# Performance work log

Measured on AMD Instinct MI355X. Metric: run time of the kernel, lower is better.

The kernel has to match this reference:

```python
import jax, jax.numpy as jnp
import numpy as np

LN_EPS = 1e-5
ATTN_THRESH = 0.0005


def _layernorm(x, g, b):
    mu = jnp.mean(x, axis=-1, keepdims=True)
    var = jnp.mean((x - mu) ** 2, axis=-1, keepdims=True)
    return (x - mu) / jnp.sqrt(var + LN_EPS) * g + b


def setup_inputs() -> dict:
    key = jax.random.key(0)
    ks = jax.random.split(key, 10)
    B, P, X, C = 4, 1024, 8192, 1024
    return {
        "feat": jax.random.normal(ks[0], (B, P, C), dtype=jnp.float32),
        "mem_k": jax.random.normal(ks[1], (B, X, C), dtype=jnp.float32),
        "mem_v": jax.random.normal(ks[2], (B, X, C), dtype=jnp.float32),
        "mem_c": jax.random.uniform(ks[3], (B, X, 1), dtype=jnp.float32),
        "mem_attn": jnp.zeros((B, X, 1), dtype=jnp.float32),
        "g_q": jax.random.uniform(ks[4], (C,), dtype=jnp.float32, minval=0.5, maxval=1.5),
        "b_q": jax.random.normal(ks[5], (C,), dtype=jnp.float32) * 0.02,
        "g_k": jax.random.uniform(ks[6], (C,), dtype=jnp.float32, minval=0.5, maxval=1.5),
        "b_k": jax.random.normal(ks[7], (C,), dtype=jnp.float32) * 0.02,
        "g_v": jax.random.uniform(ks[8], (C,), dtype=jnp.float32, minval=0.5, maxval=1.5),
        "b_v": jax.random.normal(ks[9], (C,), dtype=jnp.float32) * 0.02,
    }


def reference(feat, mem_k, mem_v, mem_c, mem_attn, g_q, b_q, g_k, b_k, g_v, b_v):
    # SpatialMemory.memory_read with res=True
    C = feat.shape[-1]
    q = _layernorm(feat, g_q, b_q)                      # [B,P,C]
    k = _layernorm(mem_k, g_k, b_k)                     # [B,X,C]
    affinity = jnp.einsum('bpc,bxc->bpx', q, k)
    affinity = affinity / jnp.sqrt(jnp.asarray(C, jnp.float32))
    # confidence scaling: mem_c viewed as [B,1,X]
    affinity = affinity * jnp.swapaxes(mem_c, 1, 2)
    attn = jax.nn.softmax(affinity, axis=-1)            # [B,P,X]
    # threshold sparsify + renormalize
    attn = jnp.where(attn < ATTN_THRESH, jnp.zeros((), attn.dtype), attn)
    attn = attn / jnp.sum(attn, axis=-1, keepdims=True)
    v = _layernorm(mem_v, g_v, b_v)                     # [B,X,C]
    out = jnp.einsum('bpx,bxc->bpc', attn, v) + feat    # residual
    return out
```

## Files before the change

### kernel.cpp

```cpp
#include <hip/hip_runtime.h>

typedef __attribute__((ext_vector_type(8))) _Float16 half8;
typedef __attribute__((ext_vector_type(4))) _Float16 half4v;
typedef __attribute__((ext_vector_type(4))) float f32x4;

__device__ __forceinline__ void gll16(const void* g, void* l) {
  __builtin_amdgcn_global_load_lds(
      (const __attribute__((address_space(1))) unsigned int*)g,
      (__attribute__((address_space(3))) unsigned int*)l, 16, 0, 0);
}

__global__ __launch_bounds__(256) void ln_fused(
    const float* __restrict__ feat, const float* __restrict__ mem_k,
    const float* __restrict__ mem_v, const float* __restrict__ g_q,
    const float* __restrict__ b_q, const float* __restrict__ g_k,
    const float* __restrict__ b_k, const float* __restrict__ g_v,
    const float* __restrict__ b_v, _Float16* __restrict__ q16,
    _Float16* __restrict__ k16, char* __restrict__ v8,
    float* __restrict__ vscale) {
  const int C = 1024;
  int wave = threadIdx.x >> 6, lane = threadIdx.x & 63;
  int task = blockIdx.x * 4 + wave;

  const float *x, *g, *b;
  int mode;
  size_t row;
  if (task < 4096) {
    x = feat; g = g_q; b = b_q; mode = 0; row = task;
  } else if (task < 36864) {
    x = mem_k; g = g_k; b = b_k; mode = 1; row = task - 4096;
  } else {
    x = mem_v; g = g_v; b = b_v; mode = 2; row = task - 36864;
  }

  const float4* xr = (const float4*)(x + row * C);
  float4 v[4];
  float s = 0.f, s2 = 0.f;
#pragma unroll
  for (int j = 0; j < 4; ++j) {
    v[j] = xr[lane + j * 64];
    s += v[j].x + v[j].y + v[j].z + v[j].w;
    s2 += v[j].x * v[j].x + v[j].y * v[j].y + v[j].z * v[j].z + v[j].w * v[j].w;
  }
#pragma unroll
  for (int off = 1; off < 64; off <<= 1) {
    s += __shfl_xor(s, off, 64);
    s2 += __shfl_xor(s2, off, 64);
  }
  float mu = s * (1.0f / C);
  float var = s2 * (1.0f / C) - mu * mu;
  float rstd = rsqrtf(var + 1e-5f);

  float y[16];
#pragma unroll
  for (int j = 0; j < 4; ++j) {
    float4 gv = ((const float4*)g)[lane + j * 64];
    float4 bv = ((const float4*)b)[lane + j * 64];
    y[4 * j + 0] = (v[j].x - mu) * rstd * gv.x + bv.x;
    y[4 * j + 1] = (v[j].y - mu) * rstd * gv.y + bv.y;
    y[4 * j + 2] = (v[j].z - mu) * rstd * gv.z + bv.z;
    y[4 * j + 3] = (v[j].w - mu) * rstd * gv.w + bv.w;
  }

  if (mode < 2) {
    _Float16* yo = (mode == 0 ? q16 : k16) + row * C;
#pragma unroll
    for (int j = 0; j < 4; ++j) {
      half4v h;
      h.x = (_Float16)y[4 * j + 0];
      h.y = (_Float16)y[4 * j + 1];
      h.z = (_Float16)y[4 * j + 2];
      h.w = (_Float16)y[4 * j + 3];
      ((half4v*)yo)[lane + j * 64] = h;
    }
  } else {
    float mx = 0.f;
#pragma unroll
    for (int i = 0; i < 16; ++i) mx = fmaxf(mx, fabsf(y[i]));
#pragma unroll
    for (int off = 1; off < 64; off <<= 1) mx = fmaxf(mx, __shfl_xor(mx, off, 64));
    mx = fmaxf(mx, 1e-20f);
    float inv = 127.0f / mx;
    unsigned* yo = (unsigned*)(v8 + row * C);
#pragma unroll
    for (int j = 0; j < 4; ++j) {
      int q0 = (int)rintf(y[4 * j + 0] * inv), q1 = (int)rintf(y[4 * j + 1] * inv);
      int q2 = (int)rintf(y[4 * j + 2] * inv), q3 = (int)rintf(y[4 * j + 3] * inv);
      unsigned pk = ((unsigned)(q0 & 0xff)) | ((unsigned)(q1 & 0xff) << 8) |
                    ((unsigned)(q2 & 0xff) << 16) | ((unsigned)(q3 & 0xff) << 24);
      yo[lane + j * 64] = pk;
    }
    if (lane == 0) vscale[row] = mx * (1.0f / 127.0f);
  }
}

__global__ __launch_bounds__(512, 2) void gemm_qk_256(
    const _Float16* __restrict__ A,
    const _Float16* __restrict__ Bm,
    _Float16* __restrict__ Sm,
    const float* __restrict__ conf)
{
  const int N = 8192, K = 1024;
  int bz = blockIdx.z;
  const _Float16* Ab = A + (size_t)bz * 1024 * K;
  const _Float16* Bb = Bm + (size_t)bz * (size_t)N * K;
  _Float16* Sb = Sm + (size_t)bz * 1024 * N;

  __shared__ _Float16 lA[4 * 8192];
  __shared__ _Float16 lB[4 * 8192];

  int tid = threadIdx.x;
  int wave = tid >> 6, lane = tid & 63;
  int wm = wave >> 2, wn = wave & 3;
  int lr = lane & 31, lk = lane >> 5;
  int m0 = blockIdx.y * 256, n0 = blockIdx.x * 256;

  typedef __attribute__((ext_vector_type(16))) float f32x16;
  f32x16 acc[4][2];
#pragma unroll
  for (int i = 0; i < 4; ++i)
#pragma unroll
    for (int j = 0; j < 2; ++j)
#pragma unroll
      for (int e = 0; e < 16; ++e) acc[i][j][e] = 0.f;

  int r = tid & 255, c0 = tid >> 8;
  const _Float16* gA = Ab + (size_t)(m0 + r) * K + c0 * 8;
  const _Float16* gB = Bb + (size_t)(n0 + r) * K + c0 * 8;
  int dA = c0 * 2048 + r * 8;

  auto stage = [&](int t) {
    int bo = (t & 3) * 8192;
    const _Float16* ga = gA + t * 32;
    const _Float16* gb = gB + t * 32;
    gll16(ga, &lA[bo + dA]);
    gll16(ga + 16, &lA[bo + dA + 4096]);
    gll16(gb, &lB[bo + dA]);
    gll16(gb + 16, &lB[bo + dA + 4096]);
  };

  auto compute = [&](int bo) {
#pragma unroll
    for (int ks = 0; ks < 2; ++ks) {
      const _Float16* la = &lA[bo + (ks * 2 + lk) * 2048 + (wm * 128 + lr) * 8];
      const _Float16* lb = &lB[bo + (ks * 2 + lk) * 2048 + (wn * 64 + lr) * 8];
      half8 a0 = *(const half8*)(la);
      half8 a1 = *(const half8*)(la + 256);
      half8 a2 = *(const half8*)(la + 512);
      half8 a3 = *(const half8*)(la + 768);
      half8 b0 = *(const half8*)(lb);
      half8 b1 = *(const half8*)(lb + 256);
      __builtin_amdgcn_s_setprio(1);
      acc[0][0] = __builtin_amdgcn_mfma_f32_32x32x16_f16(a0, b0, acc[0][0], 0, 0, 0);
      acc[1][0] = __builtin_amdgcn_mfma_f32_32x32x16_f16(a1, b0, acc[1][0], 0, 0, 0);
      acc[2][0] = __builtin_amdgcn_mfma_f32_32x32x16_f16(a2, b0, acc[2][0], 0, 0, 0);
      acc[3][0] = __builtin_amdgcn_mfma_f32_32x32x16_f16(a3, b0, acc[3][0], 0, 0, 0);
      acc[0][1] = __builtin_amdgcn_mfma_f32_32x32x16_f16(a0, b1, acc[0][1], 0, 0, 0);
      acc[1][1] = __builtin_amdgcn_mfma_f32_32x32x16_f16(a1, b1, acc[1][1], 0, 0, 0);
      acc[2][1] = __builtin_amdgcn_mfma_f32_32x32x16_f16(a2, b1, acc[2][1], 0, 0, 0);
      acc[3][1] = __builtin_amdgcn_mfma_f32_32x32x16_f16(a3, b1, acc[3][1], 0, 0, 0);
      __builtin_amdgcn_s_setprio(0);
    }
  };

  stage(0);
  stage(1);
  stage(2);

#pragma unroll 4
  for (int kt = 0; kt < 29; ++kt) {
    stage(kt + 3);
    __builtin_amdgcn_s_waitcnt(0xF7C);
    __builtin_amdgcn_s_barrier();
    __builtin_amdgcn_sched_barrier(0);
    compute((kt & 3) * 8192);
    __builtin_amdgcn_sched_barrier(0);
    __builtin_amdgcn_s_barrier();
  }
  __builtin_amdgcn_s_waitcnt(0xF78);
  __builtin_amdgcn_s_barrier();
  __builtin_amdgcn_sched_barrier(0);
  compute(1 * 8192);
  __builtin_amdgcn_sched_barrier(0);
  __builtin_amdgcn_s_barrier();
  __builtin_amdgcn_s_waitcnt(0xF74);
  __builtin_amdgcn_s_barrier();
  __builtin_amdgcn_sched_barrier(0);
  compute(2 * 8192);
  __builtin_amdgcn_sched_barrier(0);
  __builtin_amdgcn_s_barrier();
  __builtin_amdgcn_s_waitcnt(0xF70);
  __builtin_amdgcn_s_barrier();
  __builtin_amdgcn_sched_barrier(0);
  compute(3 * 8192);

  const float* cb = conf + (size_t)bz * N;
#pragma unroll
  for (int nf = 0; nf < 2; ++nf) {
    int gn = n0 + wn * 64 + nf * 32 + lr;
    float cs = 0.03125f * cb[gn];
#pragma unroll
    for (int mf = 0; mf < 4; ++mf) {
      int gmb = m0 + wm * 128 + mf * 32 + 4 * lk;
#pragma unroll
      for (int rr = 0; rr < 16; ++rr) {
        int gm = gmb + (rr & 3) + 8 * (rr >> 2);
        Sb[(size_t)gm * N + gn] = (_Float16)(acc[mf][nf][rr] * cs);
      }
    }
  }
}

__device__ __forceinline__ void acc4(float* a, unsigned w, float wt) {
  a[0] += wt * (float)(signed char)(w & 0xff);
  a[1] += wt * (float)(signed char)((w >> 8) & 0xff);
  a[2] += wt * (float)(signed char)((w >> 16) & 0xff);
  a[3] += wt * (float)(signed char)(w >> 24);
}

__global__ __launch_bounds__(512) void softmax_gather(
    const _Float16* __restrict__ S, const char* __restrict__ v8,
    const float* __restrict__ vscale, const float* __restrict__ feat,
    float* __restrict__ out) {
  const int X = 8192, C = 1024;
  int row = blockIdx.x;
  int b = row >> 10;
  int t = threadIdx.x;
  int wave = t >> 6, lane = t & 63;

  __shared__ float sh[8];
  __shared__ int scnt;
  __shared__ unsigned short sx[2048];
  __shared__ float sw[2048];
  __shared__ float red[8][1028];

  const half8* sr = (const half8*)(S + (size_t)row * X);
  float v[16];
#pragma unroll
  for (int j = 0; j < 2; ++j) {
    half8 h = sr[t + j * 512];
#pragma unroll
    for (int c = 0; c < 8; ++c) v[j * 8 + c] = (float)h[c];
  }

  float m = -1e30f;
#pragma unroll
  for (int i = 0; i < 16; ++i) m = fmaxf(m, v[i]);
#pragma unroll
  for (int off = 1; off < 64; off <<= 1) m = fmaxf(m, __shfl_xor(m, off, 64));
  if (lane == 0) sh[wave] = m;
  __syncthreads();
  m = fmaxf(fmaxf(fmaxf(sh[0], sh[1]), fmaxf(sh[2], sh[3])),
            fmaxf(fmaxf(sh[4], sh[5]), fmaxf(sh[6], sh[7])));
  __syncthreads();

  float l = 0.f;
#pragma unroll
  for (int i = 0; i < 16; ++i) {
    v[i] = __expf(v[i] - m);
    l += v[i];
  }
#pragma unroll
  for (int off = 1; off < 64; off <<= 1) l += __shfl_xor(l, off, 64);
  if (lane == 0) sh[wave] = l;
  __syncthreads();
  l = sh[0] + sh[1] + sh[2] + sh[3] + sh[4] + sh[5] + sh[6] + sh[7];
  __syncthreads();

  float thr = 0.0005f * l;
  float ks = 0.f;
#pragma unroll
  for (int i = 0; i < 16; ++i) {
    v[i] = (v[i] >= thr) ? v[i] : 0.f;
    ks += v[i];
  }
#pragma unroll
  for (int off = 1; off < 64; off <<= 1) ks += __shfl_xor(ks, off, 64);
  if (lane == 0) sh[wave] = ks;
  if (t == 0) scnt = 0;
  __syncthreads();
  ks = sh[0] + sh[1] + sh[2] + sh[3] + sh[4] + sh[5] + sh[6] + sh[7];

  float inv = 1.0f / ks;
  const float* sb = vscale + (size_t)b * X;
#pragma unroll
  for (int j = 0; j < 2; ++j) {
#pragma unroll
    for (int c = 0; c < 8; ++c) {
      float val = v[j * 8 + c];
      if (val > 0.f) {
        int pos = atomicAdd(&scnt, 1);
        int x = (t + j * 512) * 8 + c;
        sx[pos] = (unsigned short)x;
        sw[pos] = val * inv * sb[x];
      }
    }
  }
  __syncthreads();
  int cnt = scnt;

  const char* vb = v8 + (size_t)b * X * C;
  int cby = lane * 16;
  float a[16];
#pragma unroll
  for (int i = 0; i < 16; ++i) a[i] = 0.f;

#pragma unroll 2
  for (int j = wave; j < cnt; j += 8) {
    int x = sx[j];
    float w = sw[j];
    uint4 pv = *(const uint4*)(vb + (size_t)x * C + cby);
    acc4(a + 0, pv.x, w);
    acc4(a + 4, pv.y, w);
    acc4(a + 8, pv.z, w);
    acc4(a + 12, pv.w, w);
  }
  float* rp = &red[wave][cby];
#pragma unroll
  for (int i = 0; i < 16; ++i) rp[i] = a[i];
  __syncthreads();

  int p = t * 2;
  float2 f = *(const float2*)(feat + (size_t)row * C + p);
  float o0 = f.x, o1 = f.y;
#pragma unroll
  for (int ss = 0; ss < 8; ++ss) {
    o0 += red[ss][p];
    o1 += red[ss][p + 1];
  }
  float2 o = {o0, o1};
  *(float2*)(out + (size_t)row * C + p) = o;
}

extern "C" void kernel_launch(void* const* d_in, const int* in_sizes, int n_in,
                              void* d_out, int out_size, void* d_ws, size_t ws_size,
                              hipStream_t stream) {
  const int B = 4, P = 1024, X = 8192, C = 1024;
  const float* feat  = (const float*)d_in[0];
  const float* mem_k = (const float*)d_in[1];
  const float* mem_v = (const float*)d_in[2];
  const float* mem_c = (const float*)d_in[3];
  const float* g_q = (const float*)d_in[5];
  const float* b_q = (const float*)d_in[6];
  const float* g_k = (const float*)d_in[7];
  const float* b_k = (const float*)d_in[8];
  const float* g_v = (const float*)d_in[9];
  const float* b_v = (const float*)d_in[10];

  char* ws = (char*)d_ws;
  const size_t MB = 1024 * 1024;
  _Float16* q16 = (_Float16*)(ws + 0);
  _Float16* k16 = (_Float16*)(ws + 8 * MB);
  _Float16* S   = (_Float16*)(ws + 72 * MB);
  char*     v8  = (char*)(ws + 136 * MB);
  float* vscale = (float*)(ws + 168 * MB);

  ln_fused<<<(4096 + 32768 + 32768) / 4, 256, 0, stream>>>(
      feat, mem_k, mem_v, g_q, b_q, g_k, b_k, g_v, b_v, q16, k16, v8, vscale);
  gemm_qk_256<<<dim3(X / 256, P / 256, B), 512, 0, stream>>>(q16, k16, S, mem_c);
  softmax_gather<<<B * P, 512, 0, stream>>>(S, v8, vscale, feat, (float*)d_out);
}
```

Baseline: 501.1 us.

## Retile QK GEMM to 256x128 double-buffer with LDS-staged epilogue, vectorize LN stores

The QK GEMM drops from a 256x256 tile with 4-stage LDS buffering to a 256x128 tile with 2-phase double buffering. This cuts LDS use and raises the occupancy bound to 4 blocks per CU. The epilogue now stages the scaled scores through padded LDS, so global writes become coalesced 16-byte stores instead of scattered 2-byte ones. LayerNorm lanes now own 16 contiguous elements so fp16 and int8 outputs are written as wide vector stores, and the gather loop unroll goes from 2 to 4. The smaller tile reduces reuse per loaded byte, and the shallower pipeline may expose load latency.

After: 535.2 us. 6.8% more time.

```diff
diff --git a/kernel.cpp b/kernel.cpp
--- a/kernel.cpp
+++ b/kernel.cpp
@@ -1,8 +1,8 @@
 #include <hip/hip_runtime.h>
 
 typedef __attribute__((ext_vector_type(8))) _Float16 half8;
-typedef __attribute__((ext_vector_type(4))) _Float16 half4v;
 typedef __attribute__((ext_vector_type(4))) float f32x4;
+typedef __attribute__((ext_vector_type(16))) float f32x16;
 
 __device__ __forceinline__ void gll16(const void* g, void* l) {
   __builtin_amdgcn_global_load_lds(
@@ -33,12 +33,12 @@
     x = mem_v; g = g_v; b = b_v; mode = 2; row = task - 36864;
   }
 
-  const float4* xr = (const float4*)(x + row * C);
+  const float4* xr = (const float4*)(x + row * C + lane * 16);
   float4 v[4];
   float s = 0.f, s2 = 0.f;
 #pragma unroll
   for (int j = 0; j < 4; ++j) {
-    v[j] = xr[lane + j * 64];
+    v[j] = xr[j];
     s += v[j].x + v[j].y + v[j].z + v[j].w;
     s2 += v[j].x * v[j].x + v[j].y * v[j].y + v[j].z * v[j].z + v[j].w * v[j].w;
   }
@@ -51,11 +51,13 @@
   float var = s2 * (1.0f / C) - mu * mu;
   float rstd = rsqrtf(var + 1e-5f);
 
+  const float4* gr = (const float4*)(g + lane * 16);
+  const float4* br = (const float4*)(b + lane * 16);
   float y[16];
 #pragma unroll
   for (int j = 0; j < 4; ++j) {
-    float4 gv = ((const float4*)g)[lane + j * 64];
-    float4 bv = ((const float4*)b)[lane + j * 64];
+    float4 gv = gr[j];
+    float4 bv = br[j];
     y[4 * j + 0] = (v[j].x - mu) * rstd * gv.x + bv.x;
     y[4 * j + 1] = (v[j].y - mu) * rstd * gv.y + bv.y;
     y[4 * j + 2] = (v[j].z - mu) * rstd * gv.z + bv.z;
@@ -63,15 +65,13 @@
   }
 
   if (mode < 2) {
-    _Float16* yo = (mode == 0 ? q16 : k16) + row * C;
-#pragma unroll
-    for (int j = 0; j < 4; ++j) {
-      half4v h;
-      h.x = (_Float16)y[4 * j + 0];
-      h.y = (_Float16)y[4 * j + 1];
-      h.z = (_Float16)y[4 * j + 2];
-      h.w = (_Float16)y[4 * j + 3];
-      ((half4v*)yo)[lane + j * 64] = h;
+    _Float16* yo = (mode == 0 ? q16 : k16) + row * C + lane * 16;
+#pragma unroll
+    for (int j = 0; j < 2; ++j) {
+      half8 h;
+#pragma unroll
+      for (int c = 0; c < 8; ++c) h[c] = (_Float16)y[8 * j + c];
+      ((half8*)yo)[j] = h;
     }
   } else {
     float mx = 0.f;
@@ -81,20 +81,22 @@
     for (int off = 1; off < 64; off <<= 1) mx = fmaxf(mx, __shfl_xor(mx, off, 64));
     mx = fmaxf(mx, 1e-20f);
     float inv = 127.0f / mx;
-    unsigned* yo = (unsigned*)(v8 + row * C);
+    uint4 pk;
+    unsigned w[4];
 #pragma unroll
     for (int j = 0; j < 4; ++j) {
       int q0 = (int)rintf(y[4 * j + 0] * inv), q1 = (int)rintf(y[4 * j + 1] * inv);
       int q2 = (int)rintf(y[4 * j + 2] * inv), q3 = (int)rintf(y[4 * j + 3] * inv);
-      unsigned pk = ((unsigned)(q0 & 0xff)) | ((unsigned)(q1 & 0xff) << 8) |
-                    ((unsigned)(q2 & 0xff) << 16) | ((unsigned)(q3 & 0xff) << 24);
-      yo[lane + j * 64] = pk;
-    }
+      w[j] = ((unsigned)(q0 & 0xff)) | ((unsigned)(q1 & 0xff) << 8) |
+             ((unsigned)(q2 & 0xff) << 16) | ((unsigned)(q3 & 0xff) << 24);
+    }
+    pk.x = w[0]; pk.y = w[1]; pk.z = w[2]; pk.w = w[3];
+    *(uint4*)(v8 + row * C + lane * 16) = pk;
     if (lane == 0) vscale[row] = mx * (1.0f / 127.0f);
   }
 }
 
-__global__ __launch_bounds__(512, 2) void gemm_qk_256(
+__global__ __launch_bounds__(512, 4) void gemm_qk_2ph(
     const _Float16* __restrict__ A,
     const _Float16* __restrict__ Bm,
     _Float16* __restrict__ Sm,
@@ -106,109 +108,104 @@
   const _Float16* Bb = Bm + (size_t)bz * (size_t)N * K;
   _Float16* Sb = Sm + (size_t)bz * 1024 * N;
 
-  __shared__ _Float16 lA[4 * 8192];
-  __shared__ _Float16 lB[4 * 8192];
+  __shared__ _Float16 smem[16384 + 8192];
+  _Float16* lA = smem;
+  _Float16* lB = smem + 16384;
 
   int tid = threadIdx.x;
   int wave = tid >> 6, lane = tid & 63;
   int wm = wave >> 2, wn = wave & 3;
   int lr = lane & 31, lk = lane >> 5;
-  int m0 = blockIdx.y * 256, n0 = blockIdx.x * 256;
-
-  typedef __attribute__((ext_vector_type(16))) float f32x16;
-  f32x16 acc[4][2];
+  int m0 = blockIdx.y * 256, n0 = blockIdx.x * 128;
+
+  f32x16 acc[4];
 #pragma unroll
   for (int i = 0; i < 4; ++i)
 #pragma unroll
-    for (int j = 0; j < 2; ++j)
-#pragma unroll
-      for (int e = 0; e < 16; ++e) acc[i][j][e] = 0.f;
+    for (int e = 0; e < 16; ++e) acc[i][e] = 0.f;
 
   int r = tid & 255, c0 = tid >> 8;
+  int rb = tid & 127, cb = tid >> 7;
   const _Float16* gA = Ab + (size_t)(m0 + r) * K + c0 * 8;
-  const _Float16* gB = Bb + (size_t)(n0 + r) * K + c0 * 8;
-  int dA = c0 * 2048 + r * 8;
+  const _Float16* gB = Bb + (size_t)(n0 + rb) * K + cb * 8;
+  int dA0 = c0 * 2048 + r * 8, dA1 = (c0 + 2) * 2048 + r * 8;
+  int dB = cb * 1024 + rb * 8;
 
   auto stage = [&](int t) {
-    int bo = (t & 3) * 8192;
+    int pA = (t & 1) * 8192, pB = (t & 1) * 4096;
     const _Float16* ga = gA + t * 32;
-    const _Float16* gb = gB + t * 32;
-    gll16(ga, &lA[bo + dA]);
-    gll16(ga + 16, &lA[bo + dA + 4096]);
-    gll16(gb, &lB[bo + dA]);
-    gll16(gb + 16, &lB[bo + dA + 4096]);
+    gll16(ga, &lA[pA + dA0]);
+    gll16(ga + 16, &lA[pA + dA1]);
+    gll16(gB + t * 32, &lB[pB + dB]);
   };
 
-  auto compute = [&](int bo) {
+  auto compute = [&](int p) {
+    int pA = p * 8192, pB = p * 4096;
 #pragma unroll
     for (int ks = 0; ks < 2; ++ks) {
-      const _Float16* la = &lA[bo + (ks * 2 + lk) * 2048 + (wm * 128 + lr) * 8];
-      const _Float16* lb = &lB[bo + (ks * 2 + lk) * 2048 + (wn * 64 + lr) * 8];
+      const _Float16* la = &lA[pA + (ks * 2 + lk) * 2048 + (wm * 128 + lr) * 8];
+      const _Float16* lb = &lB[pB + (ks * 2 + lk) * 1024 + (wn * 32 + lr) * 8];
       half8 a0 = *(const half8*)(la);
       half8 a1 = *(const half8*)(la + 256);
       half8 a2 = *(const half8*)(la + 512);
       half8 a3 = *(const half8*)(la + 768);
       half8 b0 = *(const half8*)(lb);
-      half8 b1 = *(const half8*)(lb + 256);
       __builtin_amdgcn_s_setprio(1);
-      acc[0][0] = __builtin_amdgcn_mfma_f32_32x32x16_f16(a0, b0, acc[0][0], 0, 0, 0);
-      acc[1][0] = __builtin_amdgcn_mfma_f32_32x32x16_f16(a1, b0, acc[1][0], 0, 0, 0);
-      acc[2][0] = __builtin_amdgcn_mfma_f32_32x32x16_f16(a2, b0, acc[2][0], 0, 0, 0);
-      acc[3][0] = __builtin_amdgcn_mfma_f32_32x32x16_f16(a3, b0, acc[3][0], 0, 0, 0);
-      acc[0][1] = __builtin_amdgcn_mfma_f32_32x32x16_f16(a0, b1, acc[0][1], 0, 0, 0);
-      acc[1][1] = __builtin_amdgcn_mfma_f32_32x32x16_f16(a1, b1, acc[1][1], 0, 0, 0);
-      acc[2][1] = __builtin_amdgcn_mfma_f32_32x32x16_f16(a2, b1, acc[2][1], 0, 0, 0);
-      acc[3][1] = __builtin_amdgcn_mfma_f32_32x32x16_f16(a3, b1, acc[3][1], 0, 0, 0);
+      acc[0] = __builtin_amdgcn_mfma_f32_32x32x16_f16(a0, b0, acc[0], 0, 0, 0);
+      acc[1] = __builtin_amdgcn_mfma_f32_32x32x16_f16(a1, b0, acc[1], 0, 0, 0);
+      acc[2] = __builtin_amdgcn_mfma_f32_32x32x16_f16(a2, b0, acc[2], 0, 0, 0);
+      acc[3] = __builtin_amdgcn_mfma_f32_32x32x16_f16(a3, b0, acc[3], 0, 0, 0);
       __builtin_amdgcn_s_setprio(0);
     }
   };
 
   stage(0);
-  stage(1);
-  stage(2);
-
-#pragma unroll 4
-  for (int kt = 0; kt < 29; ++kt) {
-    stage(kt + 3);
-    __builtin_amdgcn_s_waitcnt(0xF7C);
-    __builtin_amdgcn_s_barrier();
-    __builtin_amdgcn_sched_barrier(0);
-    compute((kt & 3) * 8192);
-    __builtin_amdgcn_sched_barrier(0);
-    __builtin_amdgcn_s_barrier();
-  }
-  __builtin_amdgcn_s_waitcnt(0xF78);
-  __builtin_amdgcn_s_barrier();
-  __builtin_amdgcn_sched_barrier(0);
-  compute(1 * 8192);
-  __builtin_amdgcn_sched_barrier(0);
-  __builtin_amdgcn_s_barrier();
-  __builtin_amdgcn_s_waitcnt(0xF74);
-  __builtin_amdgcn_s_barrier();
-  __builtin_amdgcn_sched_barrier(0);
-  compute(2 * 8192);
-  __builtin_amdgcn_sched_barrier(0);
-  __builtin_amdgcn_s_barrier();
   __builtin_amdgcn_s_waitcnt(0xF70);
   __builtin_amdgcn_s_barrier();
   __builtin_amdgcn_sched_barrier(0);
-  compute(3 * 8192);
-
-  const float* cb = conf + (size_t)bz * N;
-#pragma unroll
-  for (int nf = 0; nf < 2; ++nf) {
-    int gn = n0 + wn * 64 + nf * 32 + lr;
-    float cs = 0.03125f * cb[gn];
-#pragma unroll
-    for (int mf = 0; mf < 4; ++mf) {
-      int gmb = m0 + wm * 128 + mf * 32 + 4 * lk;
-#pragma unroll
-      for (int rr = 0; rr < 16; ++rr) {
-        int gm = gmb + (rr & 3) + 8 * (rr >> 2);
-        Sb[(size_t)gm * N + gn] = (_Float16)(acc[mf][nf][rr] * cs);
-      }
-    }
-  }
+
+#pragma unroll 1
+  for (int t = 0; t < 31; ++t) {
+    stage(t + 1);
+    compute(t & 1);
+    __builtin_amdgcn_sched_barrier(0);
+    __builtin_amdgcn_s_waitcnt(0xF70);
+    __builtin_amdgcn_s_barrier();
+    __builtin_amdgcn_sched_barrier(0);
+  }
+  compute(1);
+
+  __syncthreads();
+  _Float16* ep = smem;
+  int gnl = wn * 32 + lr;
+  float cs = 0.03125f * conf[(size_t)bz * N + n0 + gnl];
+#pragma unroll 1
+  for (int h = 0; h < 2; ++h) {
+    if (wm == h) {
+#pragma unroll
+      for (int mf = 0; mf < 4; ++mf)
+#pragma unroll
+        for (int rr = 0; rr < 16; ++rr) {
+          int rloc = mf * 32 + (rr & 3) + 8 * (rr >> 2) + 4 * lk;
+          ep[rloc * 130 + gnl] = (_Float16)(acc[mf][rr] * cs);
+        }
+    }
+    __syncthreads();
+#pragma unroll
+    for (int it = 0; it < 4; ++it) {
+      int rloc = (tid >> 4) + 32 * it;
+      int ch = tid & 15;
+      half8 hv = *(const half8*)&ep[rloc * 130 + ch * 8];
+      *(half8*)&Sb[(size_t)(m0 + h * 128 + rloc) * N + n0 + ch * 8] = hv;
+    }
+    __syncthreads();
+  }
+}
+
+__device__ __forceinline__ float h2f(unsigned short hb) {
+  _Float16 h;
+  __builtin_memcpy(&h, &hb, 2);
+  return (float)h;
 }
 
 __device__ __forceinline__ void acc4(float* a, unsigned w, float wt) {
@@ -305,7 +302,7 @@
 #pragma unroll
   for (int i = 0; i < 16; ++i) a[i] = 0.f;
 
-#pragma unroll 2
+#pragma unroll 4
   for (int j = wave; j < cnt; j += 8) {
     int x = sx[j];
     float w = sw[j];
@@ -357,6 +354,6 @@
 
   ln_fused<<<(4096 + 32768 + 32768) / 4, 256, 0, stream>>>(
       feat, mem_k, mem_v, g_q, b_q, g_k, b_k, g_v, b_v, q16, k16, v8, vscale);
-  gemm_qk_256<<<dim3(X / 256, P / 256, B), 512, 0, stream>>>(q16, k16, S, mem_c);
+  gemm_qk_2ph<<<dim3(X / 128, P / 256, B), 512, 0, stream>>>(q16, k16, S, mem_c);
   softmax_gather<<<B * P, 512, 0, stream>>>(S, v8, vscale, feat, (float*)d_out);
 }
```
